# Kernel optimization log

Measured on AMD Instinct MI355X. Metric: run time of the kernel, lower is better.

## Reference

```python
import jax, jax.numpy as jnp
import numpy as np

N_BINS = 229
OUT_F = 88
MODEL = 128
W_SIZE = 30
WIN = 2 * W_SIZE + 1  # 61


def _window(spec):
    B, T, F = spec.shape
    padded = jnp.pad(spec, ((0, 0), (W_SIZE, W_SIZE), (0, 0)))
    idx = jnp.arange(T)[:, None] + jnp.arange(WIN)[None, :]
    return padded[:, idx, :]


def setup_inputs() -> dict:
    key = jax.random.key(0)
    ks = jax.random.split(key, 12)
    B, T = 4, 1024
    s = 0.05
    return {
        "spec": jax.random.normal(ks[0], (B, T, N_BINS), dtype=jnp.float32),
        # frame_stack: Linear(N_BINS -> OUT_F)
        "W_frame": jax.random.normal(ks[1], (N_BINS, OUT_F), dtype=jnp.float32) * s,
        "b_frame": jnp.zeros((OUT_F,), dtype=jnp.float32),
        # onset attention: Linear(N_BINS + N_BINS -> MODEL), v: Linear(MODEL -> 1, no bias)
        "W_attn_o": jax.random.normal(ks[2], (2 * N_BINS, MODEL), dtype=jnp.float32) * s,
        "b_attn_o": jnp.zeros((MODEL,), dtype=jnp.float32),
        "v_o": jax.random.normal(ks[3], (MODEL,), dtype=jnp.float32) * s,
        # onset linear1: Linear(N_BINS -> OUT_F)
        "W_lin1": jax.random.normal(ks[4], (N_BINS, OUT_F), dtype=jnp.float32) * s,
        "b_lin1": jnp.zeros((OUT_F,), dtype=jnp.float32),
        # combine attention: Linear(2*OUT_F + N_BINS -> MODEL)
        "W_attn_c": jax.random.normal(ks[5], (2 * OUT_F + N_BINS, MODEL), dtype=jnp.float32) * s,
        "b_attn_c": jnp.zeros((MODEL,), dtype=jnp.float32),
        "v_c": jax.random.normal(ks[6], (MODEL,), dtype=jnp.float32) * s,
        # combine linear: Linear(2*OUT_F + N_BINS -> OUT_F)
        "W_linc": jax.random.normal(ks[7], (2 * OUT_F + N_BINS, OUT_F), dtype=jnp.float32) * s,
        "b_linc": jnp.zeros((OUT_F,), dtype=jnp.float32),
    }


def _attend(hidden, win, Wa, ba, v):
    B, T, Wn, F = win.shape
    h = jnp.broadcast_to(hidden[:, :, None, :], (B, T, Wn, hidden.shape[-1]))
    energy = jnp.tanh(jnp.concatenate([h, win], axis=-1) @ Wa + ba)
    scores = energy @ v
    return jax.nn.softmax(scores, axis=-1)


def reference(spec, W_frame, b_frame, W_attn_o, b_attn_o, v_o, W_lin1, b_lin1,
              W_attn_c, b_attn_c, v_c, W_linc, b_linc):
    win = _window(spec)

    feat_pred = spec @ W_frame + b_frame  # [B,T,OUT_F]

    # Onset stack
    a_onset = _attend(spec, win, W_attn_o, b_attn_o, v_o)
    weighted_o = jnp.einsum('btw,btwf->btf', a_onset, win)  # [B,T,N_BINS]
    onset_pred = jax.nn.sigmoid(weighted_o @ W_lin1 + b_lin1)  # [B,T,OUT_F]

    # Combine stack
    x = jnp.concatenate([feat_pred, onset_pred], axis=-1)  # [B,T,2*OUT_F]
    a_frame = _attend(x, win, W_attn_c, b_attn_c, v_c)
    weighted_c = jnp.einsum('btw,btwf->btf', a_frame, win)  # [B,T,N_BINS]
    frame_pred = jax.nn.sigmoid(jnp.concatenate([x, weighted_c], axis=-1) @ W_linc + b_linc)

    return (frame_pred, a_frame[:, :, None, :], onset_pred, a_onset[:, :, None, :], feat_pred)
```

## Files before the change

### kernel.cpp

```cpp
#include <hip/hip_runtime.h>

#define NBINS 229
#define OUTF  88
#define MODEL 128
#define WSZ   30
#define WIN   61
#define TLEN  1024
#define BT    4096

#define NC1 648
#define NP1 704
#define NC2 216

typedef short bf16x8 __attribute__((ext_vector_type(8)));
typedef float f32x4 __attribute__((ext_vector_type(4)));
typedef unsigned short ushort_t;

__device__ __forceinline__ float sigmoid_f(float x) {
    return __builtin_amdgcn_rcpf(1.f + __expf(-x));
}
__device__ __forceinline__ ushort_t f2bf(float f) {
    unsigned u = __float_as_uint(f);
    return (ushort_t)((u + 0x7fffu + ((u >> 16) & 1u)) >> 16);
}

__device__ __forceinline__ float dot8(uint4 pv, float4 ha, float4 hb,
                                      float4 va, float4 vb) {
    float r;
    r  = va.x * __builtin_amdgcn_rcpf(__builtin_fmaf(ha.x, __uint_as_float(pv.x << 16), 1.f));
    r += va.y * __builtin_amdgcn_rcpf(__builtin_fmaf(ha.y, __uint_as_float(pv.x & 0xffff0000u), 1.f));
    r += va.z * __builtin_amdgcn_rcpf(__builtin_fmaf(ha.z, __uint_as_float(pv.y << 16), 1.f));
    r += va.w * __builtin_amdgcn_rcpf(__builtin_fmaf(ha.w, __uint_as_float(pv.y & 0xffff0000u), 1.f));
    r += vb.x * __builtin_amdgcn_rcpf(__builtin_fmaf(hb.x, __uint_as_float(pv.z << 16), 1.f));
    r += vb.y * __builtin_amdgcn_rcpf(__builtin_fmaf(hb.y, __uint_as_float(pv.z & 0xffff0000u), 1.f));
    r += vb.z * __builtin_amdgcn_rcpf(__builtin_fmaf(hb.z, __uint_as_float(pv.w << 16), 1.f));
    r += vb.w * __builtin_amdgcn_rcpf(__builtin_fmaf(hb.w, __uint_as_float(pv.w & 0xffff0000u), 1.f));
    return r;
}

#define PREP_BLOCKS 901

__global__ __launch_bounds__(256) void prep_kernel(
    const float* __restrict__ Wf,  const float* __restrict__ bfr,
    const float* __restrict__ Wao, const float* __restrict__ bao,
    const float* __restrict__ Wl1,
    const float* __restrict__ Wac, const float* __restrict__ bac,
    const float* __restrict__ Wlc,
    const float* __restrict__ vo, const float* __restrict__ vc,
    ushort_t* __restrict__ B1b, ushort_t* __restrict__ B2b,
    float* __restrict__ bias1, float* __restrict__ bias2,
    float* __restrict__ sv)
{
    __shared__ float red[4];
    const int b = blockIdx.x;
    if (b < 704) {
        int idx = b * 256 + threadIdx.x;
        int n = idx >> 8, k = idx & 255;
        float v = 0.f;
        if (k < NBINS && n < NC1) {
            if (n < 88)       v = Wf[k * 88 + n];
            else if (n < 216) v = Wao[k * MODEL + (n - 88)];
            else if (n < 344) v = Wao[(k + NBINS) * MODEL + (n - 216)];
            else if (n < 472) v = Wac[(k + 176) * MODEL + (n - 344)];
            else if (n < 560) v = Wl1[k * 88 + (n - 472)];
            else              v = Wlc[(k + 176) * 88 + (n - 560)];
        }
        B1b[idx] = f2bf(v);
    } else if (b < 896) {
        int idx = (b - 704) * 256 + threadIdx.x;
        int n = idx / 192, k = idx - n * 192;
        float v = 0.f;
        if (k < 176 && n < NC2)
            v = (n < 128) ? Wac[k * MODEL + n] : Wlc[k * 88 + (n - 128)];
        B2b[idx] = f2bf(v);
    } else if (b < 900) {
        int idx = (b - 896) * 256 + threadIdx.x;
        if (idx < 704)
            bias1[idx] = (idx < 88) ? bfr[idx] : (idx < 216 ? bao[idx - 88] : 0.f);
        else if (idx < 960) {
            int n = idx - 704;
            bias2[n] = (n < 128) ? bac[n] : 0.f;
        }
    } else {
        int wid = threadIdx.x >> 6, lane = threadIdx.x & 63;
        const float* vp = (wid < 2) ? vo : vc;
        float val = vp[(wid & 1) * 64 + lane];
#pragma unroll
        for (int m = 32; m; m >>= 1) val += __shfl_xor(val, m, 64);
        if (lane == 0) red[wid] = val;
        __syncthreads();
        if (threadIdx.x == 0) {
            sv[0] = red[0] + red[1];
            sv[1] = red[2] + red[3];
        }
    }
}

__device__ __forceinline__ bf16x8 cvt8(f32x4 a, f32x4 b) {
    bf16x8 r;
    r[0] = (short)f2bf(a.x); r[1] = (short)f2bf(a.y);
    r[2] = (short)f2bf(a.z); r[3] = (short)f2bf(a.w);
    r[4] = (short)f2bf(b.x); r[5] = (short)f2bf(b.y);
    r[6] = (short)f2bf(b.z); r[7] = (short)f2bf(b.w);
    return r;
}
__device__ __forceinline__ bf16x8 loadA(const float* sp, int k0) {
    if (k0 > 228) return (bf16x8)(short)0;
    f32x4 a, b;
    __builtin_memcpy(&a, sp + k0, 16);
    if (k0 <= 216) {
        __builtin_memcpy(&b, sp + k0 + 4, 16);
    } else {
        b = (f32x4){sp[228], 0.f, 0.f, 0.f};
    }
    return cvt8(a, b);
}

template<int KITER, int RTS>
__global__ __launch_bounds__(256) void gemm_mfma(
    const float* __restrict__ spec,
    const ushort_t* __restrict__ Bb,
    const float* __restrict__ bias, int Nc,
    float* __restrict__ feat, float* __restrict__ EHo_,
    ushort_t* __restrict__ EPo_, ushort_t* __restrict__ EPc_,
    ushort_t* __restrict__ Rb_, ushort_t* __restrict__ Qb_)
{
    const int tid = threadIdx.x;
    const int wv = tid >> 6, ln = tid & 63;
    const int l15 = ln & 15, qd = ln >> 4;
    const int flat = blockIdx.y * gridDim.x + blockIdx.x;
    const int e = flat & 7, kf = flat >> 3;
    const int rb = (e * (1 << RTS) + (kf & ((1 << RTS) - 1))) * 64;
    const int cb = (kf >> RTS) * 64;
    const int lkb = KITER * 32;

    const float* sp = spec + (size_t)(rb + wv * 16 + l15) * NBINS;
    const ushort_t* bp[4];
#pragma unroll
    for (int nt = 0; nt < 4; nt++)
        bp[nt] = Bb + (size_t)(cb + nt * 16 + l15) * lkb + qd * 8;

    f32x4 acc[4];
#pragma unroll
    for (int nt = 0; nt < 4; nt++) acc[nt] = (f32x4){0.f, 0.f, 0.f, 0.f};

    bf16x8 af = loadA(sp, qd * 8), bfv[4];
#pragma unroll
    for (int nt = 0; nt < 4; nt++) bfv[nt] = *(const bf16x8*)bp[nt];

    for (int it = 0; it < KITER; it++) {
        bf16x8 an, bn[4];
        const int nk = (it + 1 < KITER) ? (it + 1) * 32 : 0;
        an = loadA(sp, nk + qd * 8);
#pragma unroll
        for (int nt = 0; nt < 4; nt++) bn[nt] = *(const bf16x8*)(bp[nt] + nk);
#pragma unroll
        for (int nt = 0; nt < 4; nt++)
            acc[nt] = __builtin_amdgcn_mfma_f32_16x16x32_bf16(
                af, bfv[nt], acc[nt], 0, 0, 0);
        af = an;
#pragma unroll
        for (int nt = 0; nt < 4; nt++) bfv[nt] = bn[nt];
    }

    const int mbase = rb + wv * 16 + qd * 4;
#pragma unroll
    for (int nt = 0; nt < 4; nt++) {
        const int n = cb + nt * 16 + l15;
        if (n < Nc) {
            const float bn = bias[n];
#pragma unroll
            for (int r = 0; r < 4; r++) {
                const int m = mbase + r;
                float val = acc[nt][r] + bn;
                if (n < 88) {
                    feat[(size_t)m * 88 + n] = val;
                } else if (n < 216) {
                    EHo_[(size_t)m * 128 + (n - 88)] = __expf(val + val);
                } else if (n < 344) {
                    EPo_[(size_t)m * 128 + (n - 216)] = f2bf(__expf(val + val));
                } else if (n < 472) {
                    EPc_[(size_t)m * 128 + (n - 344)] = f2bf(__expf(val + val));
                } else if (n < 560) {
                    Rb_[(size_t)m * 96 + (n - 472)] = f2bf(val);
                } else {
                    Qb_[(size_t)m * 96 + (n - 560)] = f2bf(val);
                }
            }
        }
    }
}

#define EPST 136
#define RST  96
#define XST  200

__global__ __launch_bounds__(512) void attn_fused(
    const float* __restrict__ EHo,
    const ushort_t* __restrict__ EPo_g,
    const ushort_t* __restrict__ Rb,
    const ushort_t* __restrict__ EPc_g,
    const ushort_t* __restrict__ Qb,
    const float* __restrict__ feat,
    const ushort_t* __restrict__ B2b,
    const float* __restrict__ bias2,
    const float* __restrict__ vo, const float* __restrict__ vc,
    const float* __restrict__ svp,
    const float* __restrict__ bl1, const float* __restrict__ blc,
    float* __restrict__ a_o_out, float* __restrict__ onset_out,
    float* __restrict__ a_c_out, float* __restrict__ frame_out)
{
    __shared__ alignas(16) ushort_t Plo[68 * EPST];
    __shared__ alignas(16) ushort_t Rl [68 * RST];
    __shared__ alignas(16) ushort_t Plc[68 * EPST];
    __shared__ alignas(16) ushort_t Ql [68 * RST];
    __shared__ alignas(16) ushort_t Xb [16 * XST];
    __shared__ alignas(16) float    EHc[8 * 128];
    __shared__ alignas(16) float    basec[8 * 88];

    const int tid = threadIdx.x;
    const int s0 = ((blockIdx.x & 7) * 64 + (blockIdx.x >> 3)) * 8;
    const int t0 = s0 & (TLEN - 1);

    for (int i = tid; i < 68 * 16; i += 512) {
        int j = i >> 4, c = (i & 15) * 8;
        int cs = ((i & 15) ^ ((j >> 3) & 7)) * 8;
        int tg = t0 + j - WSZ;
        uint4 vP = {0x3f803f80u, 0x3f803f80u, 0x3f803f80u, 0x3f803f80u};
        uint4 vC = vP;
        if ((unsigned)tg < (unsigned)TLEN) {
            vP = *(const uint4*)&EPo_g[(size_t)(s0 - WSZ + j) * 128 + c];
            vC = *(const uint4*)&EPc_g[(size_t)(s0 - WSZ + j) * 128 + c];
        }
        *(uint4*)&Plo[j * EPST + cs] = vP;
        *(uint4*)&Plc[j * EPST + cs] = vC;
    }
    for (int i = tid; i < 68 * 12; i += 512) {
        int j = i / 12, c = (i - j * 12) * 8;
        int tg = t0 + j - WSZ;
        uint4 vR = {0u, 0u, 0u, 0u}, vQ = {0u, 0u, 0u, 0u};
        if ((unsigned)tg < (unsigned)TLEN) {
            vR = *(const uint4*)&Rb[(size_t)(s0 - WSZ + j) * 96 + c];
            vQ = *(const uint4*)&Qb[(size_t)(s0 - WSZ + j) * 96 + c];
        }
        *(uint4*)&Rl[j * RST + c] = vR;
        *(uint4*)&Ql[j * RST + c] = vQ;
    }
    for (int i = tid; i < 16 * XST; i += 512) {
        int r = i / XST, k = i - r * XST;
        ushort_t v = 0;
        if (r < 8 && k < 88) v = f2bf(feat[(size_t)(s0 + r) * 88 + k]);
        Xb[i] = v;
    }
    __syncthreads();

    const int q = tid >> 6;
    const int w = tid & 63;
    const int s = s0 + q;
    const int su = __builtin_amdgcn_readfirstlane(s);
    const int row = q + ((w < WIN) ? w : 0);
    const int rsw = (row >> 3) & 7;

    {
        const ushort_t* pb = &Plo[row * EPST];
        const float* hrow = EHo + (size_t)su * 128;
        float accr = 0.f;
#pragma unroll
        for (int d8 = 0; d8 < 16; d8++) {
            uint4 pv = *(const uint4*)(pb + ((d8 ^ rsw) << 3));
            float4 ha = *(const float4*)(hrow + d8 * 8);
            float4 hb = *(const float4*)(hrow + d8 * 8 + 4);
            float4 va = *(const float4*)(vo + d8 * 8);
            float4 vb = *(const float4*)(vo + d8 * 8 + 4);
            accr += dot8(pv, ha, hb, va, vb);
        }
        float eng = svp[0] - 2.f * accr;
        if (w >= WIN) eng = -1e30f;

        float mx = eng;
#pragma unroll
        for (int m = 32; m; m >>= 1) mx = fmaxf(mx, __shfl_xor(mx, m, 64));
        float ex = __expf(eng - mx);
        float sm = ex;
#pragma unroll
        for (int m = 32; m; m >>= 1) sm += __shfl_xor(sm, m, 64);
        float a = ex * __builtin_amdgcn_rcpf(sm);
        if (w < WIN) a_o_out[(size_t)s * WIN + w] = a;

        if (w < 44) {
            const int f = 2 * w;
            float acc0 = bl1[f], acc1 = bl1[f + 1];
            const ushort_t* rr0 = &Rl[q * RST + f];
#pragma unroll
            for (int ww = 0; ww < WIN; ww++) {
                float aw = __uint_as_float(
                    __builtin_amdgcn_readlane(__float_as_uint(a), ww));
                unsigned u = *(const unsigned*)(rr0 + ww * RST);
                acc0 += aw * __uint_as_float(u << 16);
                acc1 += aw * __uint_as_float(u & 0xffff0000u);
            }
            float p0 = sigmoid_f(acc0), p1 = sigmoid_f(acc1);
            *(float2*)&onset_out[(size_t)s * OUTF + f] = make_float2(p0, p1);
            ushort2 o; o.x = f2bf(p0); o.y = f2bf(p1);
            *(ushort2*)&Xb[q * XST + 88 + f] = o;
        }
    }
    __syncthreads();

    {
        const int l15 = w & 15, qd = w >> 4;
#pragma unroll
        for (int rt = 0; rt < 2; rt++) {
            const int t = q + rt * 8;
            if (t < 14) {
                const int n0 = t * 16;
                const ushort_t* bp = B2b + (size_t)(n0 + l15) * 192 + qd * 8;
                const ushort_t* ap = &Xb[l15 * XST + qd * 8];
                f32x4 acc = (f32x4){0.f, 0.f, 0.f, 0.f};
#pragma unroll
                for (int it = 0; it < 6; it++) {
                    bf16x8 av = *(const bf16x8*)(ap + it * 32);
                    bf16x8 bv = *(const bf16x8*)(bp + it * 32);
                    acc = __builtin_amdgcn_mfma_f32_16x16x32_bf16(
                        av, bv, acc, 0, 0, 0);
                }
                if (qd < 2) {
                    const int n = n0 + l15;
                    const float b2 = bias2[n];
#pragma unroll
                    for (int r = 0; r < 4; r++) {
                        const int m = qd * 4 + r;
                        float val = acc[r] + b2;
                        if (n < 128)        EHc[m * 128 + n] = __expf(val + val);
                        else if (n < NC2)   basec[m * 88 + (n - 128)] = val;
                    }
                }
            }
        }
    }
    __syncthreads();

    {
        const ushort_t* pb = &Plc[row * EPST];
        const float* hl = &EHc[q * 128];
        float accr = 0.f;
#pragma unroll
        for (int d8 = 0; d8 < 16; d8++) {
            uint4 pv = *(const uint4*)(pb + ((d8 ^ rsw) << 3));
            float4 ha = *(const float4*)(hl + d8 * 8);
            float4 hb = *(const float4*)(hl + d8 * 8 + 4);
            float4 va = *(const float4*)(vc + d8 * 8);
            float4 vb = *(const float4*)(vc + d8 * 8 + 4);
            accr += dot8(pv, ha, hb, va, vb);
        }
        float eng = svp[1] - 2.f * accr;
        if (w >= WIN) eng = -1e30f;

        float mx = eng;
#pragma unroll
        for (int m = 32; m; m >>= 1) mx = fmaxf(mx, __shfl_xor(mx, m, 64));
        float ex = __expf(eng - mx);
        float sm = ex;
#pragma unroll
        for (int m = 32; m; m >>= 1) sm += __shfl_xor(sm, m, 64);
        float a = ex * __builtin_amdgcn_rcpf(sm);
        if (w < WIN) a_c_out[(size_t)s * WIN + w] = a;

        if (w < 44) {
            const int f = 2 * w;
            float acc0 = blc[f]     + basec[q * 88 + f];
            float acc1 = blc[f + 1] + basec[q * 88 + f + 1];
            const ushort_t* rr0 = &Ql[q * RST + f];
#pragma unroll
            for (int ww = 0; ww < WIN; ww++) {
                float aw = __uint_as_float(
                    __builtin_amdgcn_readlane(__float_as_uint(a), ww));
                unsigned u = *(const unsigned*)(rr0 + ww * RST);
                acc0 += aw * __uint_as_float(u << 16);
                acc1 += aw * __uint_as_float(u & 0xffff0000u);
            }
            float p0 = sigmoid_f(acc0), p1 = sigmoid_f(acc1);
            *(float2*)&frame_out[(size_t)s * OUTF + f] = make_float2(p0, p1);
        }
    }
}

extern "C" void kernel_launch(void* const* d_in, const int* in_sizes, int n_in,
                              void* d_out, int out_size, void* d_ws, size_t ws_size,
                              hipStream_t stream)
{
    const float* spec = (const float*)d_in[0];
    const float* Wf   = (const float*)d_in[1];
    const float* bf_  = (const float*)d_in[2];
    const float* Wao  = (const float*)d_in[3];
    const float* bao  = (const float*)d_in[4];
    const float* vo   = (const float*)d_in[5];
    const float* Wl1  = (const float*)d_in[6];
    const float* bl1  = (const float*)d_in[7];
    const float* Wac  = (const float*)d_in[8];
    const float* bac  = (const float*)d_in[9];
    const float* vc   = (const float*)d_in[10];
    const float* Wlc  = (const float*)d_in[11];
    const float* blc  = (const float*)d_in[12];

    float* out  = (float*)d_out;
    float* out0 = out;
    float* out1 = out + 360448;
    float* out2 = out + 610304;
    float* out3 = out + 970752;
    float* out4 = out + 1220608;

    float* ws = (float*)d_ws;
    float*    sv    = ws;
    float*    bias1 = ws + 16;
    float*    bias2 = ws + 720;
    ushort_t* B1b   = (ushort_t*)(ws + 976);
    ushort_t* B2b   = (ushort_t*)(ws + 91088);
    float*    EHo   = ws + 115664;
    ushort_t* EPo   = (ushort_t*)(ws + 639952);
    ushort_t* EPc   = (ushort_t*)(ws + 902096);
    ushort_t* Rb    = (ushort_t*)(ws + 1164240);
    ushort_t* Qb    = (ushort_t*)(ws + 1360848);
    (void)ws_size; (void)in_sizes; (void)n_in; (void)out_size;

    prep_kernel<<<PREP_BLOCKS, 256, 0, stream>>>(
        Wf, bf_, Wao, bao, Wl1, Wac, bac, Wlc, vo, vc,
        B1b, B2b, bias1, bias2, sv);

    gemm_mfma<8, 3><<<dim3(NP1 / 64, 64), 256, 0, stream>>>(
        spec, B1b, bias1, NC1, out4, EHo, EPo, EPc, Rb, Qb);

    attn_fused<<<BT / 8, 512, 0, stream>>>(
        EHo, EPo, Rb, EPc, Qb, out4, B2b, bias2, vo, vc, sv, bl1, blc,
        out3, out2, out1, out0);
}
```

Measured before the change: 123.5 us.

## Fuse weight prep into GEMM with LDS-staged B tiles; drop softmax max

Merges the separate weight-conversion kernel into the GEMM kernel. Each GEMM block now converts its own 64-column slice of the fp32 weights to bf16 in swizzled shared memory, which removes one launch and the global B1b round trip. B2b, bias2 and sv prep run in extra blocks of the same grid, ordered before the attention kernel. The softmax max-reduction is also dropped and exp is taken directly, which relies on the energies staying bounded. Each GEMM block now does strided fp32 weight reads redundantly, and overflow is possible if scores grow large.

Result: faster. 115.8 us (-6.3%).

```diff
diff --git a/kernel.cpp b/kernel.cpp
--- a/kernel.cpp
+++ b/kernel.cpp
@@ -38,64 +38,6 @@
     return r;
 }
 
-#define PREP_BLOCKS 901
-
-__global__ __launch_bounds__(256) void prep_kernel(
-    const float* __restrict__ Wf,  const float* __restrict__ bfr,
-    const float* __restrict__ Wao, const float* __restrict__ bao,
-    const float* __restrict__ Wl1,
-    const float* __restrict__ Wac, const float* __restrict__ bac,
-    const float* __restrict__ Wlc,
-    const float* __restrict__ vo, const float* __restrict__ vc,
-    ushort_t* __restrict__ B1b, ushort_t* __restrict__ B2b,
-    float* __restrict__ bias1, float* __restrict__ bias2,
-    float* __restrict__ sv)
-{
-    __shared__ float red[4];
-    const int b = blockIdx.x;
-    if (b < 704) {
-        int idx = b * 256 + threadIdx.x;
-        int n = idx >> 8, k = idx & 255;
-        float v = 0.f;
-        if (k < NBINS && n < NC1) {
-            if (n < 88)       v = Wf[k * 88 + n];
-            else if (n < 216) v = Wao[k * MODEL + (n - 88)];
-            else if (n < 344) v = Wao[(k + NBINS) * MODEL + (n - 216)];
-            else if (n < 472) v = Wac[(k + 176) * MODEL + (n - 344)];
-            else if (n < 560) v = Wl1[k * 88 + (n - 472)];
-            else              v = Wlc[(k + 176) * 88 + (n - 560)];
-        }
-        B1b[idx] = f2bf(v);
-    } else if (b < 896) {
-        int idx = (b - 704) * 256 + threadIdx.x;
-        int n = idx / 192, k = idx - n * 192;
-        float v = 0.f;
-        if (k < 176 && n < NC2)
-            v = (n < 128) ? Wac[k * MODEL + n] : Wlc[k * 88 + (n - 128)];
-        B2b[idx] = f2bf(v);
-    } else if (b < 900) {
-        int idx = (b - 896) * 256 + threadIdx.x;
-        if (idx < 704)
-            bias1[idx] = (idx < 88) ? bfr[idx] : (idx < 216 ? bao[idx - 88] : 0.f);
-        else if (idx < 960) {
-            int n = idx - 704;
-            bias2[n] = (n < 128) ? bac[n] : 0.f;
-        }
-    } else {
-        int wid = threadIdx.x >> 6, lane = threadIdx.x & 63;
-        const float* vp = (wid < 2) ? vo : vc;
-        float val = vp[(wid & 1) * 64 + lane];
-#pragma unroll
-        for (int m = 32; m; m >>= 1) val += __shfl_xor(val, m, 64);
-        if (lane == 0) red[wid] = val;
-        __syncthreads();
-        if (threadIdx.x == 0) {
-            sv[0] = red[0] + red[1];
-            sv[1] = red[2] + red[3];
-        }
-    }
-}
-
 __device__ __forceinline__ bf16x8 cvt8(f32x4 a, f32x4 b) {
     bf16x8 r;
     r[0] = (short)f2bf(a.x); r[1] = (short)f2bf(a.y);
@@ -116,77 +58,129 @@
     return cvt8(a, b);
 }
 
-template<int KITER, int RTS>
-__global__ __launch_bounds__(256) void gemm_mfma(
+#define GP_BLOCKS 897
+
+__global__ __launch_bounds__(256) void gemm_prep(
     const float* __restrict__ spec,
-    const ushort_t* __restrict__ Bb,
-    const float* __restrict__ bias, int Nc,
+    const float* __restrict__ Wf,  const float* __restrict__ bfr,
+    const float* __restrict__ Wao, const float* __restrict__ bao,
+    const float* __restrict__ Wl1,
+    const float* __restrict__ Wac, const float* __restrict__ bac,
+    const float* __restrict__ Wlc,
+    const float* __restrict__ vo,  const float* __restrict__ vc,
     float* __restrict__ feat, float* __restrict__ EHo_,
     ushort_t* __restrict__ EPo_, ushort_t* __restrict__ EPc_,
-    ushort_t* __restrict__ Rb_, ushort_t* __restrict__ Qb_)
+    ushort_t* __restrict__ Rb_,  ushort_t* __restrict__ Qb_,
+    ushort_t* __restrict__ B2b, float* __restrict__ bias2,
+    float* __restrict__ sv)
 {
+    __shared__ ushort_t B1t[64 * 256];
+    __shared__ float red[4];
     const int tid = threadIdx.x;
-    const int wv = tid >> 6, ln = tid & 63;
-    const int l15 = ln & 15, qd = ln >> 4;
-    const int flat = blockIdx.y * gridDim.x + blockIdx.x;
-    const int e = flat & 7, kf = flat >> 3;
-    const int rb = (e * (1 << RTS) + (kf & ((1 << RTS) - 1))) * 64;
-    const int cb = (kf >> RTS) * 64;
-    const int lkb = KITER * 32;
-
-    const float* sp = spec + (size_t)(rb + wv * 16 + l15) * NBINS;
-    const ushort_t* bp[4];
-#pragma unroll
-    for (int nt = 0; nt < 4; nt++)
-        bp[nt] = Bb + (size_t)(cb + nt * 16 + l15) * lkb + qd * 8;
-
-    f32x4 acc[4];
-#pragma unroll
-    for (int nt = 0; nt < 4; nt++) acc[nt] = (f32x4){0.f, 0.f, 0.f, 0.f};
-
-    bf16x8 af = loadA(sp, qd * 8), bfv[4];
-#pragma unroll
-    for (int nt = 0; nt < 4; nt++) bfv[nt] = *(const bf16x8*)bp[nt];
-
-    for (int it = 0; it < KITER; it++) {
-        bf16x8 an, bn[4];
-        const int nk = (it + 1 < KITER) ? (it + 1) * 32 : 0;
-        an = loadA(sp, nk + qd * 8);
-#pragma unroll
-        for (int nt = 0; nt < 4; nt++) bn[nt] = *(const bf16x8*)(bp[nt] + nk);
-#pragma unroll
-        for (int nt = 0; nt < 4; nt++)
-            acc[nt] = __builtin_amdgcn_mfma_f32_16x16x32_bf16(
-                af, bfv[nt], acc[nt], 0, 0, 0);
-        af = an;
-#pragma unroll
-        for (int nt = 0; nt < 4; nt++) bfv[nt] = bn[nt];
-    }
-
-    const int mbase = rb + wv * 16 + qd * 4;
-#pragma unroll
-    for (int nt = 0; nt < 4; nt++) {
-        const int n = cb + nt * 16 + l15;
-        if (n < Nc) {
-            const float bn = bias[n];
-#pragma unroll
-            for (int r = 0; r < 4; r++) {
-                const int m = mbase + r;
-                float val = acc[nt][r] + bn;
-                if (n < 88) {
-                    feat[(size_t)m * 88 + n] = val;
-                } else if (n < 216) {
-                    EHo_[(size_t)m * 128 + (n - 88)] = __expf(val + val);
-                } else if (n < 344) {
-                    EPo_[(size_t)m * 128 + (n - 216)] = f2bf(__expf(val + val));
-                } else if (n < 472) {
-                    EPc_[(size_t)m * 128 + (n - 344)] = f2bf(__expf(val + val));
-                } else if (n < 560) {
-                    Rb_[(size_t)m * 96 + (n - 472)] = f2bf(val);
-                } else {
-                    Qb_[(size_t)m * 96 + (n - 560)] = f2bf(val);
+    const int b = blockIdx.x;
+
+    if (b < 704) {
+        const int e = b & 7, kf = b >> 3;
+        const int rb = (e * 8 + (kf & 7)) * 64;
+        const int cb = (kf >> 3) * 64;
+
+        {
+            const int n  = tid & 63;
+            const int kq = tid >> 6;
+            const int ng = cb + n;
+            const float* srcp = nullptr; int sstr = 0;
+            if (ng < 88)       { srcp = Wf  + ng;                          sstr = 88;  }
+            else if (ng < 216) { srcp = Wao + (ng - 88);                   sstr = 128; }
+            else if (ng < 344) { srcp = Wao + (size_t)NBINS * 128 + (ng - 216); sstr = 128; }
+            else if (ng < 472) { srcp = Wac + (size_t)176 * 128 + (ng - 344);   sstr = 128; }
+            else if (ng < 560) { srcp = Wl1 + (ng - 472);                  sstr = 88;  }
+            else if (ng < NC1) { srcp = Wlc + (size_t)176 * 88 + (ng - 560);    sstr = 88; }
+            const int n31 = n & 31;
+#pragma unroll
+            for (int it = 0; it < 8; it++) {
+                const int k8 = kq * 8 + it * 32;
+                bf16x8 vv;
+#pragma unroll
+                for (int j = 0; j < 8; j++) {
+                    const int k = k8 + j;
+                    float v = (srcp && k < NBINS) ? srcp[(size_t)k * sstr] : 0.f;
+                    vv[j] = (short)f2bf(v);
                 }
-            }
+                const int chunk = (kq + 4 * it) ^ n31;
+                *(bf16x8*)&B1t[n * 256 + chunk * 8] = vv;
+            }
+        }
+        __syncthreads();
+
+        const int wv = tid >> 6, ln = tid & 63;
+        const int l15 = ln & 15, qd = ln >> 4;
+        const float* sp = spec + (size_t)(rb + wv * 16 + l15) * NBINS;
+
+        f32x4 acc[4];
+#pragma unroll
+        for (int nt = 0; nt < 4; nt++) acc[nt] = (f32x4){0.f, 0.f, 0.f, 0.f};
+
+        bf16x8 af = loadA(sp, qd * 8);
+#pragma unroll
+        for (int it = 0; it < 8; it++) {
+            const int nk = (it + 1 < 8) ? (it + 1) * 32 : 0;
+            bf16x8 an = loadA(sp, nk + qd * 8);
+            const int cq = qd + 4 * it;
+#pragma unroll
+            for (int nt = 0; nt < 4; nt++) {
+                const int nn = nt * 16 + l15;
+                bf16x8 bv = *(const bf16x8*)&B1t[nn * 256 + ((cq ^ (nn & 31)) << 3)];
+                acc[nt] = __builtin_amdgcn_mfma_f32_16x16x32_bf16(
+                    af, bv, acc[nt], 0, 0, 0);
+            }
+            af = an;
+        }
+
+        const int mbase = rb + wv * 16 + qd * 4;
+#pragma unroll
+        for (int nt = 0; nt < 4; nt++) {
+            const int n = cb + nt * 16 + l15;
+            if (n < NC1) {
+                const float bn = (n < 88) ? bfr[n] : (n < 216 ? bao[n - 88] : 0.f);
+#pragma unroll
+                for (int r = 0; r < 4; r++) {
+                    const int m = mbase + r;
+                    float val = acc[nt][r] + bn;
+                    if (n < 88) {
+                        feat[(size_t)m * 88 + n] = val;
+                    } else if (n < 216) {
+                        EHo_[(size_t)m * 128 + (n - 88)] = __expf(val + val);
+                    } else if (n < 344) {
+                        EPo_[(size_t)m * 128 + (n - 216)] = f2bf(__expf(val + val));
+                    } else if (n < 472) {
+                        EPc_[(size_t)m * 128 + (n - 344)] = f2bf(__expf(val + val));
+                    } else if (n < 560) {
+                        Rb_[(size_t)m * 96 + (n - 472)] = f2bf(val);
+                    } else {
+                        Qb_[(size_t)m * 96 + (n - 560)] = f2bf(val);
+                    }
+                }
+            }
+        }
+    } else if (b < 896) {
+        int idx = (b - 704) * 256 + tid;
+        int n = idx / 192, k = idx - n * 192;
+        float v = 0.f;
+        if (k < 176 && n < NC2)
+            v = (n < 128) ? Wac[k * MODEL + n] : Wlc[k * 88 + (n - 128)];
+        B2b[idx] = f2bf(v);
+    } else {
+        bias2[tid] = (tid < 128) ? bac[tid] : 0.f;
+        int wid = tid >> 6, lane = tid & 63;
+        const float* vp = (wid < 2) ? vo : vc;
+        float val = vp[(wid & 1) * 64 + lane];
+#pragma unroll
+        for (int m = 32; m; m >>= 1) val += __shfl_xor(val, m, 64);
+        if (lane == 0) red[wid] = val;
+        __syncthreads();
+        if (tid == 0) {
+            sv[0] = red[0] + red[1];
+            sv[1] = red[2] + red[3];
         }
     }
 }
@@ -275,12 +269,7 @@
             accr += dot8(pv, ha, hb, va, vb);
         }
         float eng = svp[0] - 2.f * accr;
-        if (w >= WIN) eng = -1e30f;
-
-        float mx = eng;
-#pragma unroll
-        for (int m = 32; m; m >>= 1) mx = fmaxf(mx, __shfl_xor(mx, m, 64));
-        float ex = __expf(eng - mx);
+        float ex = (w < WIN) ? __expf(eng) : 0.f;
         float sm = ex;
 #pragma unroll
         for (int m = 32; m; m >>= 1) sm += __shfl_xor(sm, m, 64);
@@ -354,12 +343,7 @@
             accr += dot8(pv, ha, hb, va, vb);
         }
         float eng = svp[1] - 2.f * accr;
-        if (w >= WIN) eng = -1e30f;
-
-        float mx = eng;
-#pragma unroll
-        for (int m = 32; m; m >>= 1) mx = fmaxf(mx, __shfl_xor(mx, m, 64));
-        float ex = __expf(eng - mx);
+        float ex = (w < WIN) ? __expf(eng) : 0.f;
         float sm = ex;
 #pragma unroll
         for (int m = 32; m; m >>= 1) sm += __shfl_xor(sm, m, 64);
@@ -412,23 +396,18 @@
 
     float* ws = (float*)d_ws;
     float*    sv    = ws;
-    float*    bias1 = ws + 16;
-    float*    bias2 = ws + 720;
-    ushort_t* B1b   = (ushort_t*)(ws + 976);
-    ushort_t* B2b   = (ushort_t*)(ws + 91088);
-    float*    EHo   = ws + 115664;
-    ushort_t* EPo   = (ushort_t*)(ws + 639952);
-    ushort_t* EPc   = (ushort_t*)(ws + 902096);
-    ushort_t* Rb    = (ushort_t*)(ws + 1164240);
-    ushort_t* Qb    = (ushort_t*)(ws + 1360848);
+    float*    bias2 = ws + 16;
+    ushort_t* B2b   = (ushort_t*)(ws + 272);
+    float*    EHo   = ws + 24848;
+    ushort_t* EPo   = (ushort_t*)(ws + 549136);
+    ushort_t* EPc   = (ushort_t*)(ws + 811280);
+    ushort_t* Rb    = (ushort_t*)(ws + 1073424);
+    ushort_t* Qb    = (ushort_t*)(ws + 1270032);
     (void)ws_size; (void)in_sizes; (void)n_in; (void)out_size;
 
-    prep_kernel<<<PREP_BLOCKS, 256, 0, stream>>>(
-        Wf, bf_, Wao, bao, Wl1, Wac, bac, Wlc, vo, vc,
-        B1b, B2b, bias1, bias2, sv);
-
-    gemm_mfma<8, 3><<<dim3(NP1 / 64, 64), 256, 0, stream>>>(
-        spec, B1b, bias1, NC1, out4, EHo, EPo, EPc, Rb, Qb);
+    gemm_prep<<<GP_BLOCKS, 256, 0, stream>>>(
+        spec, Wf, bf_, Wao, bao, Wl1, Wac, bac, Wlc, vo, vc,
+        out4, EHo, EPo, EPc, Rb, Qb, B2b, bias2, sv);
 
     attn_fused<<<BT / 8, 512, 0, stream>>>(
         EHo, EPo, Rb, EPc, Qb, out4, B2b, bias2, vo, vc, sv, bl1, blc,
```
